# Kernel optimization log

Measured on AMD Instinct MI355X. Metric: run time of the kernel, lower is better.

Reference implementation:

```python
import jax, jax.numpy as jnp
import numpy as np

B = 64        # graphs in batch
N = 2048      # nodes per graph (uniform -> static pooled sizes)
DEG = 16      # avg degree
E = B * N * DEG
F0 = 128      # node feature dim


def setup_inputs() -> dict:
    key = jax.random.key(0)
    ks = jax.random.split(key, 24)
    x = jax.random.normal(ks[0], (B * N, F0), dtype=jnp.float32)
    # within-graph random edges, PyG batched-graph layout (contiguous node blocks)
    loc = jax.random.randint(ks[1], (2, B, N * DEG), 0, N)
    off = (jnp.arange(B, dtype=jnp.int32) * N)[:, None]
    src = (loc[0].astype(jnp.int32) + off).reshape(-1)
    dst = (loc[1].astype(jnp.int32) + off).reshape(-1)
    g = lambda i, shp: jax.random.normal(ks[i], shp, dtype=jnp.float32) * 0.05
    return {
        'x': x, 'src': src, 'dst': dst,
        'w1l': g(2, (128, 128)), 'b1': jnp.zeros((128,), jnp.float32), 'w1r': g(3, (128, 128)), 'pw1': g(4, (128,)),
        'w2l': g(5, (128, 128)), 'b2': jnp.zeros((128,), jnp.float32), 'w2r': g(6, (128, 128)), 'pw2': g(7, (128,)),
        'w3l': g(8, (128, 128)), 'b3': jnp.zeros((128,), jnp.float32), 'w3r': g(9, (128, 128)), 'pw3': g(10, (128,)),
        'l1w': g(11, (256, 128)), 'l1b': jnp.zeros((128,), jnp.float32),
        'l2w': g(12, (128, 64)), 'l2b': jnp.zeros((64,), jnp.float32),
        'l3w': g(13, (64, 2)), 'l3b': jnp.zeros((2,), jnp.float32),
    }


def _sage(x, src, dst, em, n_nodes, Wl, b, Wr):
    # PyG SAGEConv: lin_l(mean_{j->i} x_j) + lin_r(x_i); edge mask zeroes dropped edges
    msg = x[src] * em[:, None]                                   # [E, F] gather
    agg = jax.ops.segment_sum(msg, dst, num_segments=n_nodes)
    cnt = jax.ops.segment_sum(em, dst, num_segments=n_nodes)
    mean = agg / jnp.maximum(cnt, 1.0)[:, None]
    return mean @ Wl + b + x @ Wr


def _topk_pool(x, src, dst, em, b_graphs, n_per, w):
    # PyG TopKPooling (min_score=None): score = tanh(x@w/||w||), keep top ratio per graph,
    # gate kept features by score, drop edges touching removed nodes, relabel.
    score = jnp.tanh((x @ w) / jnp.linalg.norm(w))
    k = n_per // 2                                               # ratio = 0.5
    _, idx = jax.lax.top_k(score.reshape(b_graphs, n_per), k)    # per-graph local idx
    perm = (jnp.arange(b_graphs, dtype=jnp.int32)[:, None] * n_per + idx.astype(jnp.int32)).reshape(-1)
    xn = x[perm] * score[perm][:, None]
    ntot = b_graphs * n_per
    kept = jnp.zeros((ntot,), bool).at[perm].set(True)
    newidx = jnp.zeros((ntot,), jnp.int32).at[perm].set(jnp.arange(b_graphs * k, dtype=jnp.int32))
    emn = em * kept[src].astype(em.dtype) * kept[dst].astype(em.dtype)
    return xn, newidx[src], newidx[dst], emn, k


def _readout(x, b_graphs, n_per):
    r = x.reshape(b_graphs, n_per, -1)
    return jnp.concatenate([r.max(axis=1), r.mean(axis=1)], axis=1)  # [B, 2F]


def _forward(x, src, dst, w1l, b1, w1r, pw1, w2l, b2, w2r, pw2, w3l, b3, w3r, pw3,
             l1w, l1b, l2w, l2b, l3w, l3b):
    em = jnp.ones((src.shape[0],), x.dtype)
    n = N
    h = jax.nn.relu(_sage(x, src, dst, em, B * n, w1l, b1, w1r))
    h, src, dst, em, n = _topk_pool(h, src, dst, em, B, n, pw1)
    x1 = _readout(h, B, n)
    h = jax.nn.relu(_sage(h, src, dst, em, B * n, w2l, b2, w2r))
    h, src, dst, em, n = _topk_pool(h, src, dst, em, B, n, pw2)
    x2 = _readout(h, B, n)
    h = jax.nn.relu(_sage(h, src, dst, em, B * n, w3l, b3, w3r))
    h, src, dst, em, n = _topk_pool(h, src, dst, em, B, n, pw3)
    x3 = _readout(h, B, n)
    z = x1 + x2 + x3
    z = jax.nn.relu(z @ l1w + l1b)            # dropout is identity in eval mode
    z = jax.nn.relu(z @ l2w + l2b)
    z = z @ l3w + l3b
    return jax.nn.log_softmax(z, axis=-1)


def reference(x, src, dst, w1l, b1, w1r, pw1, w2l, b2, w2r, pw2, w3l, b3, w3r, pw3,
              l1w, l1b, l2w, l2b, l3w, l3b):
    return _forward(x, src, dst, w1l, b1, w1r, pw1, w2l, b2, w2r, pw2, w3l, b3, w3r, pw3,
                    l1w, l1b, l2w, l2b, l3w, l3b)
```

## Files before the change

kernel.cpp:

```cpp
#include <hip/hip_runtime.h>
#include <cmath>

#define NT1  131072
#define ETOT 2097152
#define NB   64
#define F    128
#define CPAD 32
#define MAXBLK 32

typedef float floatx4 __attribute__((ext_vector_type(4)));

__global__ void hist_kernel(const int* __restrict__ dst, int* __restrict__ deg) {
  int e = blockIdx.x * blockDim.x + threadIdx.x;
  if (e < ETOT) atomicAdd(&deg[dst[e]], 1);
}

__global__ void scan1_kernel(const int* __restrict__ deg, int* __restrict__ rowstart,
                             int* __restrict__ bsum) {
  __shared__ int ls[256];
  int base = blockIdx.x * 1024;
  int t = threadIdx.x;
  int i = base + t * 4;
  int a0 = deg[i], a1 = deg[i + 1], a2 = deg[i + 2], a3 = deg[i + 3];
  int s = a0 + a1 + a2 + a3;
  ls[t] = s;
  __syncthreads();
  for (int off = 1; off < 256; off <<= 1) {
    int v = (t >= off) ? ls[t - off] : 0;
    __syncthreads();
    ls[t] += v;
    __syncthreads();
  }
  int excl = ls[t] - s;
  rowstart[i]     = excl;
  rowstart[i + 1] = excl + a0;
  rowstart[i + 2] = excl + a0 + a1;
  rowstart[i + 3] = excl + a0 + a1 + a2;
  if (t == 255) bsum[blockIdx.x] = ls[255];
}

__global__ void scan2_kernel(int* __restrict__ bsum) {
  __shared__ int ls[128];
  int t = threadIdx.x;
  int v0 = bsum[t];
  ls[t] = v0;
  __syncthreads();
  for (int off = 1; off < 128; off <<= 1) {
    int v = (t >= off) ? ls[t - off] : 0;
    __syncthreads();
    ls[t] += v;
    __syncthreads();
  }
  bsum[t] = ls[t] - v0;
}

__global__ void scan3_kernel(int* __restrict__ rowstart, const int* __restrict__ bsum,
                             int* __restrict__ cursor) {
  int base = blockIdx.x * 1024;
  int off = bsum[blockIdx.x];
  int i = base + threadIdx.x * 4;
  int r0 = rowstart[i] + off, r1 = rowstart[i + 1] + off;
  int r2 = rowstart[i + 2] + off, r3 = rowstart[i + 3] + off;
  rowstart[i] = r0; rowstart[i + 1] = r1; rowstart[i + 2] = r2; rowstart[i + 3] = r3;
  cursor[i] = r0; cursor[i + 1] = r1; cursor[i + 2] = r2; cursor[i + 3] = r3;
}

__global__ void fill_kernel(const int* __restrict__ src, const int* __restrict__ dst,
                            int* __restrict__ cursor, int* __restrict__ csr) {
  int e = blockIdx.x * blockDim.x + threadIdx.x;
  if (e < ETOT) {
    int pos = atomicAdd(&cursor[dst[e]], 1);
    csr[pos] = src[e];
  }
}

__global__ void init_id_kernel(int* __restrict__ m, int* __restrict__ orig,
                               const int* __restrict__ rowstart,
                               const int* __restrict__ deg, int2* __restrict__ sd2) {
  int v = blockIdx.x * blockDim.x + threadIdx.x;
  m[v] = v; orig[v] = v;
  sd2[v] = make_int2(rowstart[v], deg[v]);
}

template <int MAP>
__global__ __launch_bounds__(256) void agg_kernel(
    const float* __restrict__ xin, const int* __restrict__ ids,
    const int* __restrict__ m, const int2* __restrict__ sd2,
    float* __restrict__ agg, const float* __restrict__ pw,
    float* __restrict__ invn) {
  if (blockIdx.x == 0 && threadIdx.x < 64) {
    int l = threadIdx.x;
    float vv = pw[l] * pw[l] + pw[l + 64] * pw[l + 64];
    #pragma unroll
    for (int o = 32; o; o >>= 1) vv += __shfl_xor(vv, o);
    if (l == 0) *invn = 1.0f / sqrtf(vv);
  }
  int swz = gridDim.x >> 3;
  int nb  = (blockIdx.x & 7) * swz + (blockIdx.x >> 3);
  int g = threadIdx.x >> 5, l = threadIdx.x & 31;
  int jd = nb * 8 + g;
  int2 sdv = sd2[jd];
  int s = sdv.x, d = sdv.y;
  float4 acc = make_float4(0.f, 0.f, 0.f, 0.f);
  int c = 0;
  for (int base = 0; base < d; base += 32) {
    int dc = min(32, d - base);
    int nbid = -1;
    if (l < dc) {
      int e = __builtin_nontemporal_load(&ids[s + base + l]);
      nbid = MAP ? m[e] : e;
    }
    int j = 0;
    for (; j + 4 <= dc; j += 4) {
      int n0 = __shfl(nbid, j, 32);
      int n1 = __shfl(nbid, j + 1, 32);
      int n2 = __shfl(nbid, j + 2, 32);
      int n3 = __shfl(nbid, j + 3, 32);
      float4 v0 = *(const float4*)(xin + (size_t)max(n0, 0) * F + l * 4);
      float4 v1 = *(const float4*)(xin + (size_t)max(n1, 0) * F + l * 4);
      float4 v2 = *(const float4*)(xin + (size_t)max(n2, 0) * F + l * 4);
      float4 v3 = *(const float4*)(xin + (size_t)max(n3, 0) * F + l * 4);
      if (n0 >= 0) { acc.x += v0.x; acc.y += v0.y; acc.z += v0.z; acc.w += v0.w; ++c; }
      if (n1 >= 0) { acc.x += v1.x; acc.y += v1.y; acc.z += v1.z; acc.w += v1.w; ++c; }
      if (n2 >= 0) { acc.x += v2.x; acc.y += v2.y; acc.z += v2.z; acc.w += v2.w; ++c; }
      if (n3 >= 0) { acc.x += v3.x; acc.y += v3.y; acc.z += v3.z; acc.w += v3.w; ++c; }
    }
    for (; j < dc; ++j) {
      int n0 = __shfl(nbid, j, 32);
      if (n0 >= 0) {
        float4 v0 = *(const float4*)(xin + (size_t)n0 * F + l * 4);
        acc.x += v0.x; acc.y += v0.y; acc.z += v0.z; acc.w += v0.w; ++c;
      }
    }
  }
  float inv = 1.0f / (float)max(c, 1);
  floatx4 o;
  o.x = acc.x * inv; o.y = acc.y * inv; o.z = acc.z * inv; o.w = acc.w * inv;
  __builtin_nontemporal_store(o, (floatx4*)(agg + (size_t)jd * F + l * 4));
}

template <int BM>
__global__ __launch_bounds__(256) void sage_gemm(
    const float* agg, const float* __restrict__ x,
    const float* __restrict__ Wl, const float* __restrict__ Wr,
    const float* __restrict__ bias, float* h,
    const float* __restrict__ pw, const float* __restrict__ invn,
    float* __restrict__ score) {
  constexpr int RQ = BM / 64;
  __shared__ float At[16][BM + 4];
  __shared__ float Wt[16][132];
  int t  = threadIdx.x;
  int tx = t & 15, ty = t >> 4;
  int i0 = blockIdx.x * BM;
  int arow, akc;
  if (BM == 128) { arow = t & 127; akc = (t >> 7) * 8; }
  else           { arow = t & 63;  akc = (t >> 6) * 4; }
  int wkr = t >> 4, wc0 = (t & 15) * 8;

  float4 va0, va1, vw0, vw1;
  auto loadT = [&](int ktile) {
    const float* Asrc = (ktile < 8) ? agg : x;
    int acol = (ktile & 7) * 16 + akc;
    const float* pA = Asrc + (size_t)(i0 + arow) * F + acol;
    va0 = *(const float4*)pA;
    if (BM == 128) va1 = *(const float4*)(pA + 4);
    const float* Wsrc = ((ktile < 8) ? Wl : Wr) + (size_t)((ktile & 7) * 16 + wkr) * F + wc0;
    vw0 = *(const float4*)Wsrc;
    vw1 = *(const float4*)(Wsrc + 4);
  };

  float acc[4 * RQ][8];
  #pragma unroll
  for (int r = 0; r < 4 * RQ; ++r)
    #pragma unroll
    for (int c = 0; c < 8; ++c) acc[r][c] = 0.f;

  loadT(0);
  for (int kt = 0; kt < 16; ++kt) {
    At[akc + 0][arow] = va0.x; At[akc + 1][arow] = va0.y;
    At[akc + 2][arow] = va0.z; At[akc + 3][arow] = va0.w;
    if (BM == 128) {
      At[akc + 4][arow] = va1.x; At[akc + 5][arow] = va1.y;
      At[akc + 6][arow] = va1.z; At[akc + 7][arow] = va1.w;
    }
    *(float4*)(&Wt[wkr][wc0]) = vw0;
    *(float4*)(&Wt[wkr][wc0 + 4]) = vw1;
    __syncthreads();
    if (kt < 15) loadT(kt + 1);
    #pragma unroll
    for (int k = 0; k < 16; ++k) {
      float4 a0 = *(float4*)(&At[k][ty * 4]);
      float4 w0 = *(float4*)(&Wt[k][tx * 4]);
      float4 w1 = *(float4*)(&Wt[k][64 + tx * 4]);
      float wr[8] = {w0.x, w0.y, w0.z, w0.w, w1.x, w1.y, w1.z, w1.w};
      float ar0[4] = {a0.x, a0.y, a0.z, a0.w};
      #pragma unroll
      for (int r = 0; r < 4; ++r)
        #pragma unroll
        for (int c = 0; c < 8; ++c)
          acc[r][c] += ar0[r] * wr[c];
      if (RQ == 2) {
        float4 a1 = *(float4*)(&At[k][64 + ty * 4]);
        float ar1[4] = {a1.x, a1.y, a1.z, a1.w};
        #pragma unroll
        for (int r = 0; r < 4; ++r)
          #pragma unroll
          for (int c = 0; c < 8; ++c)
            acc[4 + r][c] += ar1[r] * wr[c];
      }
    }
    __syncthreads();
  }

  float4 bb0 = *(const float4*)(bias + tx * 4);
  float4 bb1 = *(const float4*)(bias + 64 + tx * 4);
  float4 pw0 = *(const float4*)(pw + tx * 4);
  float4 pw1 = *(const float4*)(pw + 64 + tx * 4);
  float inorm = *invn;
  #pragma unroll
  for (int r = 0; r < 4 * RQ; ++r) {
    int row = i0 + ((r < 4) ? (ty * 4 + r) : (64 + ty * 4 + r - 4));
    float4 o0, o1;
    o0.x = fmaxf(acc[r][0] + bb0.x, 0.f);
    o0.y = fmaxf(acc[r][1] + bb0.y, 0.f);
    o0.z = fmaxf(acc[r][2] + bb0.z, 0.f);
    o0.w = fmaxf(acc[r][3] + bb0.w, 0.f);
    o1.x = fmaxf(acc[r][4] + bb1.x, 0.f);
    o1.y = fmaxf(acc[r][5] + bb1.y, 0.f);
    o1.z = fmaxf(acc[r][6] + bb1.z, 0.f);
    o1.w = fmaxf(acc[r][7] + bb1.w, 0.f);
    *(float4*)(h + (size_t)row * F + tx * 4) = o0;
    *(float4*)(h + (size_t)row * F + 64 + tx * 4) = o1;
    float p = o0.x * pw0.x + o0.y * pw0.y + o0.z * pw0.z + o0.w * pw0.w
            + o1.x * pw1.x + o1.y * pw1.y + o1.z * pw1.z + o1.w * pw1.w;
    #pragma unroll
    for (int off = 8; off; off >>= 1) p += __shfl_xor(p, off);
    if (tx == 0) score[row] = tanhf(p * inorm);
  }
}

__global__ __launch_bounds__(256) void topk_kernel(
    const float* __restrict__ score, float* __restrict__ thr,
    int* __restrict__ quota, int* __restrict__ tiecur,
    int* __restrict__ curg, int nper, int k) {
  __shared__ unsigned su[2048];
  __shared__ int hist[256];
  __shared__ int vsel;
  int b = blockIdx.x, t = threadIdx.x;
  for (int i = t; i < nper; i += 256) {
    unsigned u = __float_as_uint(score[b * nper + i]);
    su[i] = (u & 0x80000000u) ? ~u : (u | 0x80000000u);
  }
  __syncthreads();
  unsigned prefix = 0;
  int rem = k;
  for (int shift = 24; shift >= 0; shift -= 8) {
    hist[t] = 0;
    __syncthreads();
    unsigned maskhi = (shift == 24) ? 0u : (0xFFFFFFFFu << (shift + 8));
    for (int i = t; i < nper; i += 256) {
      unsigned u = su[i];
      if ((u & maskhi) == prefix) atomicAdd(&hist[(u >> shift) & 255], 1);
    }
    __syncthreads();
    for (int off = 1; off < 256; off <<= 1) {
      int v = (t + off < 256) ? hist[t + off] : 0;
      __syncthreads();
      hist[t] += v;
      __syncthreads();
    }
    if (hist[t] >= rem && (t == 255 || hist[t + 1] < rem)) vsel = t;
    __syncthreads();
    int v = vsel;
    int above = (v == 255) ? 0 : hist[v + 1];
    rem -= above;
    prefix |= ((unsigned)v << shift);
    __syncthreads();
  }
  if (t == 0) {
    unsigned s = prefix;
    unsigned ub = (s >> 31) ? (s & 0x7FFFFFFFu) : ~s;
    thr[b] = __uint_as_float(ub);
    quota[b] = rem;
    tiecur[b * CPAD] = 0; curg[b * CPAD] = 0;
  }
}

__global__ __launch_bounds__(256) void select_kernel(
    const float* __restrict__ h, const float* __restrict__ score,
    const float* __restrict__ thr, const int* __restrict__ quota,
    int* __restrict__ tiecur, int* __restrict__ curg,
    const int* __restrict__ origA, int* __restrict__ origB,
    int* __restrict__ m, float* __restrict__ xnext,
    const int* __restrict__ rowstart, const int* __restrict__ deg,
    int2* __restrict__ sd2, float* __restrict__ pmax, float* __restrict__ psum,
    int nper, int k) {
  __shared__ int   snid[64];
  __shared__ float ssc[64];
  __shared__ float smax[8][128], ssum[8][128];
  int t = threadIdx.x;
  int base = blockIdx.x * 64;
  int b = base / nper;
  if (t < 64) {
    int i = base + t;
    float sc = score[i];
    float T = thr[b];
    int keep = (sc > T) ? 1 : 0;
    if (!keep && sc == T) keep = (atomicAdd(&tiecur[b * CPAD], 1) < quota[b]) ? 1 : 0;
    unsigned long long mask = __ballot(keep);
    int pre = __popcll(mask & ((1ull << t) - 1ull));
    int tot = __popcll(mask);
    int wbase = 0;
    if (t == 0 && tot) wbase = atomicAdd(&curg[b * CPAD], tot);
    wbase = __shfl(wbase, 0);
    int nid = keep ? (b * k + wbase + pre) : -1;
    int orig = origA[i];
    m[orig] = nid;
    if (nid >= 0) {
      origB[nid] = orig;
      sd2[nid] = make_int2(rowstart[orig], deg[orig]);
    }
    snid[t] = nid; ssc[t] = sc;
  }
  __syncthreads();
  int g = t >> 5, l32 = t & 31;
  float4 pm = make_float4(-INFINITY, -INFINITY, -INFINITY, -INFINITY);
  float4 ps = make_float4(0.f, 0.f, 0.f, 0.f);
  for (int n = g; n < 64; n += 8) {
    int nid = snid[n];
    if (nid >= 0) {
      float sc = ssc[n];
      float4 v = *(const float4*)(h + (size_t)(base + n) * F + l32 * 4);
      v.x *= sc; v.y *= sc; v.z *= sc; v.w *= sc;
      *(float4*)(xnext + (size_t)nid * F + l32 * 4) = v;
      pm.x = fmaxf(pm.x, v.x); pm.y = fmaxf(pm.y, v.y);
      pm.z = fmaxf(pm.z, v.z); pm.w = fmaxf(pm.w, v.w);
      ps.x += v.x; ps.y += v.y; ps.z += v.z; ps.w += v.w;
    }
  }
  *(float4*)(&smax[g][l32 * 4]) = pm;
  *(float4*)(&ssum[g][l32 * 4]) = ps;
  __syncthreads();
  if (t < 128) {
    float mx = -INFINITY, sm = 0.f;
    #pragma unroll
    for (int gg = 0; gg < 8; ++gg) {
      mx = fmaxf(mx, smax[gg][t]);
      sm += ssum[gg][t];
    }
    int nblk = nper >> 6;
    int blkpos = blockIdx.x - b * nblk;
    int o = (b * MAXBLK + blkpos) * 128 + t;
    pmax[o] = mx; psum[o] = sm;
  }
}

__global__ void readout_final(const float* __restrict__ pmax,
                              const float* __restrict__ psum,
                              float* __restrict__ z, int k, int nblk) {
  int b = blockIdx.x, f = threadIdx.x;
  float mx = -INFINITY, sm = 0.f;
  for (int ch = 0; ch < nblk; ++ch) {
    int o = (b * MAXBLK + ch) * 128 + f;
    mx = fmaxf(mx, pmax[o]);
    sm += psum[o];
  }
  z[b * 256 + f]       += mx;
  z[b * 256 + 128 + f] += sm / (float)k;
}

__global__ void mlp_kernel(const float* __restrict__ z,
                           const float* __restrict__ l1w, const float* __restrict__ l1b,
                           const float* __restrict__ l2w, const float* __restrict__ l2b,
                           const float* __restrict__ l3w, const float* __restrict__ l3b,
                           float* __restrict__ out) {
  int b = blockIdx.x, t = threadIdx.x;
  __shared__ float zz[256], o1[128], o2[64], lg[2];
  zz[t]       = z[b * 256 + t];
  zz[t + 128] = z[b * 256 + 128 + t];
  __syncthreads();
  float a = l1b[t];
  for (int i = 0; i < 256; ++i) a += zz[i] * l1w[i * 128 + t];
  o1[t] = fmaxf(a, 0.f);
  __syncthreads();
  if (t < 64) {
    float a2 = l2b[t];
    for (int i = 0; i < 128; ++i) a2 += o1[i] * l2w[i * 64 + t];
    o2[t] = fmaxf(a2, 0.f);
  }
  __syncthreads();
  if (t < 2) {
    float a3 = l3b[t];
    for (int i = 0; i < 64; ++i) a3 += o2[i] * l3w[i * 2 + t];
    lg[t] = a3;
  }
  __syncthreads();
  if (t == 0) {
    float mmax = fmaxf(lg[0], lg[1]);
    float lse = mmax + logf(expf(lg[0] - mmax) + expf(lg[1] - mmax));
    out[b * 2 + 0] = lg[0] - lse;
    out[b * 2 + 1] = lg[1] - lse;
  }
}

extern "C" void kernel_launch(void* const* d_in, const int* in_sizes, int n_in,
                              void* d_out, int out_size, void* d_ws, size_t ws_size,
                              hipStream_t stream) {
  const float* x   = (const float*)d_in[0];
  const int*   src = (const int*)d_in[1];
  const int*   dst = (const int*)d_in[2];
  const float* Wl[3] = {(const float*)d_in[3], (const float*)d_in[7],  (const float*)d_in[11]};
  const float* bs[3] = {(const float*)d_in[4], (const float*)d_in[8],  (const float*)d_in[12]};
  const float* Wr[3] = {(const float*)d_in[5], (const float*)d_in[9],  (const float*)d_in[13]};
  const float* pw[3] = {(const float*)d_in[6], (const float*)d_in[10], (const float*)d_in[14]};
  const float* l1w = (const float*)d_in[15]; const float* l1b = (const float*)d_in[16];
  const float* l2w = (const float*)d_in[17]; const float* l2b = (const float*)d_in[18];
  const float* l3w = (const float*)d_in[19]; const float* l3b = (const float*)d_in[20];
  float* out = (float*)d_out;

  char* p = (char*)d_ws;
  auto take = [&](size_t bytes) { char* q = p; p += (bytes + 255) & ~(size_t)255; return q; };
  float* aggh   = (float*)take((size_t)NT1 * F * 4);
  float* xbuf   = (float*)take((size_t)65536 * F * 4);
  float* score  = (float*)take((size_t)NT1 * 4);
  int* deg      = (int*)take((size_t)NT1 * 4);
  int* rowstart = (int*)take((size_t)NT1 * 4);
  int* cursor   = (int*)take((size_t)NT1 * 4);
  int* m        = (int*)take((size_t)NT1 * 4);
  int* origA    = (int*)take((size_t)NT1 * 4);
  int* origB    = (int*)take((size_t)NT1 * 4);
  int2* sd2     = (int2*)take((size_t)NT1 * 8);
  int* csr      = (int*)take((size_t)ETOT * 4);
  int* bsum     = (int*)take(128 * 4);
  float* thr    = (float*)take(NB * 4);
  int* quota    = (int*)take(NB * 4);
  int* tiecur   = (int*)take(NB * CPAD * 4);
  int* curg     = (int*)take(NB * CPAD * 4);
  float* z      = (float*)take(NB * 256 * 4);
  float* pmax   = (float*)take((size_t)NB * MAXBLK * F * 4);
  float* psum   = (float*)take((size_t)NB * MAXBLK * F * 4);
  float* invn   = (float*)take(4);

  hipMemsetAsync(deg, 0, (size_t)NT1 * 4, stream);
  hipMemsetAsync(z, 0, (size_t)NB * 256 * 4, stream);

  hist_kernel<<<ETOT / 256, 256, 0, stream>>>(dst, deg);
  scan1_kernel<<<128, 256, 0, stream>>>(deg, rowstart, bsum);
  scan2_kernel<<<1, 128, 0, stream>>>(bsum);
  scan3_kernel<<<128, 256, 0, stream>>>(rowstart, bsum, cursor);
  fill_kernel<<<ETOT / 256, 256, 0, stream>>>(src, dst, cursor, csr);
  init_id_kernel<<<NT1 / 256, 256, 0, stream>>>(m, origA, rowstart, deg, sd2);

  int NT = NT1, nper = 2048;
  const float* xin = x;
  int* oin = origA; int* oout = origB;
  for (int s = 0; s < 3; ++s) {
    int k = nper / 2;
    if (s == 0)
      agg_kernel<0><<<NT / 8, 256, 0, stream>>>(xin, csr, m, sd2, aggh, pw[s], invn);
    else
      agg_kernel<1><<<NT / 8, 256, 0, stream>>>(xin, csr, m, sd2, aggh, pw[s], invn);
    if (s == 0)
      sage_gemm<128><<<NT / 128, 256, 0, stream>>>(aggh, xin, Wl[s], Wr[s], bs[s], aggh,
                                                   pw[s], invn, score);
    else
      sage_gemm<64><<<NT / 64, 256, 0, stream>>>(aggh, xin, Wl[s], Wr[s], bs[s], aggh,
                                                 pw[s], invn, score);
    topk_kernel<<<NB, 256, 0, stream>>>(score, thr, quota, tiecur, curg, nper, k);
    select_kernel<<<NT / 64, 256, 0, stream>>>(aggh, score, thr, quota, tiecur, curg,
                                               oin, oout, m, xbuf, rowstart, deg, sd2,
                                               pmax, psum, nper, k);
    readout_final<<<NB, 128, 0, stream>>>(pmax, psum, z, k, nper >> 6);
    NT = NB * k; nper = k; xin = xbuf;
    int* tmp = oin; oin = oout; oout = tmp;
  }
  mlp_kernel<<<NB, 128, 0, stream>>>(z, l1w, l1b, l2w, l2b, l3w, l3b, out);
}
```

Before: 709.1 us.

## Unroll neighbor gather by eight and drop register prefetch in SAGE GEMM

The mean-aggregation kernel gains an 8-wide unrolled gather loop so more independent feature-row loads are in flight per warp. Its final store goes back to a plain cached store instead of a nontemporal one. The SAGE GEMM drops its software register prefetch of the next k-tile and instead loads each tile at the top of its iteration, with the barrier moved before the shared-memory write. This lowers register pressure in the GEMM, but global-load latency is no longer hidden behind the previous tile's compute.

New measurement: 690.0 us. 2.7% less time.

```diff
diff --git a/kernel.cpp b/kernel.cpp
--- a/kernel.cpp
+++ b/kernel.cpp
@@ -7,8 +7,6 @@
 #define F    128
 #define CPAD 32
 #define MAXBLK 32
-
-typedef float floatx4 __attribute__((ext_vector_type(4)));
 
 __global__ void hist_kernel(const int* __restrict__ dst, int* __restrict__ deg) {
   int e = blockIdx.x * blockDim.x + threadIdx.x;
@@ -111,6 +109,18 @@
       nbid = MAP ? m[e] : e;
     }
     int j = 0;
+    for (; j + 8 <= dc; j += 8) {
+      int n[8];
+      float4 v[8];
+      #pragma unroll
+      for (int q = 0; q < 8; ++q) n[q] = __shfl(nbid, j + q, 32);
+      #pragma unroll
+      for (int q = 0; q < 8; ++q)
+        v[q] = *(const float4*)(xin + (size_t)max(n[q], 0) * F + l * 4);
+      #pragma unroll
+      for (int q = 0; q < 8; ++q)
+        if (n[q] >= 0) { acc.x += v[q].x; acc.y += v[q].y; acc.z += v[q].z; acc.w += v[q].w; ++c; }
+    }
     for (; j + 4 <= dc; j += 4) {
       int n0 = __shfl(nbid, j, 32);
       int n1 = __shfl(nbid, j + 1, 32);
@@ -134,9 +144,8 @@
     }
   }
   float inv = 1.0f / (float)max(c, 1);
-  floatx4 o;
-  o.x = acc.x * inv; o.y = acc.y * inv; o.z = acc.z * inv; o.w = acc.w * inv;
-  __builtin_nontemporal_store(o, (floatx4*)(agg + (size_t)jd * F + l * 4));
+  acc.x *= inv; acc.y *= inv; acc.z *= inv; acc.w *= inv;
+  *(float4*)(agg + (size_t)jd * F + l * 4) = acc;
 }
 
 template <int BM>
@@ -157,26 +166,23 @@
   else           { arow = t & 63;  akc = (t >> 6) * 4; }
   int wkr = t >> 4, wc0 = (t & 15) * 8;
 
-  float4 va0, va1, vw0, vw1;
-  auto loadT = [&](int ktile) {
-    const float* Asrc = (ktile < 8) ? agg : x;
-    int acol = (ktile & 7) * 16 + akc;
-    const float* pA = Asrc + (size_t)(i0 + arow) * F + acol;
-    va0 = *(const float4*)pA;
-    if (BM == 128) va1 = *(const float4*)(pA + 4);
-    const float* Wsrc = ((ktile < 8) ? Wl : Wr) + (size_t)((ktile & 7) * 16 + wkr) * F + wc0;
-    vw0 = *(const float4*)Wsrc;
-    vw1 = *(const float4*)(Wsrc + 4);
-  };
-
   float acc[4 * RQ][8];
   #pragma unroll
   for (int r = 0; r < 4 * RQ; ++r)
     #pragma unroll
     for (int c = 0; c < 8; ++c) acc[r][c] = 0.f;
 
-  loadT(0);
   for (int kt = 0; kt < 16; ++kt) {
+    const float* Asrc = (kt < 8) ? agg : x;
+    int acol = (kt & 7) * 16 + akc;
+    const float* pA = Asrc + (size_t)(i0 + arow) * F + acol;
+    float4 va0 = *(const float4*)pA;
+    float4 va1;
+    if (BM == 128) va1 = *(const float4*)(pA + 4);
+    const float* Wsrc = ((kt < 8) ? Wl : Wr) + (size_t)((kt & 7) * 16 + wkr) * F + wc0;
+    float4 vw0 = *(const float4*)Wsrc;
+    float4 vw1 = *(const float4*)(Wsrc + 4);
+    __syncthreads();
     At[akc + 0][arow] = va0.x; At[akc + 1][arow] = va0.y;
     At[akc + 2][arow] = va0.z; At[akc + 3][arow] = va0.w;
     if (BM == 128) {
@@ -186,7 +192,6 @@
     *(float4*)(&Wt[wkr][wc0]) = vw0;
     *(float4*)(&Wt[wkr][wc0 + 4]) = vw1;
     __syncthreads();
-    if (kt < 15) loadT(kt + 1);
     #pragma unroll
     for (int k = 0; k < 16; ++k) {
       float4 a0 = *(float4*)(&At[k][ty * 4]);
@@ -209,7 +214,6 @@
             acc[4 + r][c] += ar1[r] * wr[c];
       }
     }
-    __syncthreads();
   }
 
   float4 bb0 = *(const float4*)(bias + tx * 4);
```
